# Kernel tuning notes

Hardware: AMD Instinct MI355X
Metric: run time of the kernel (lower is better)

The kernel has to match this reference:

```python
import jax, jax.numpy as jnp
import numpy as np

D = 256      # d_model
NH = 8       # num_heads
NP = 4       # n_points
H = 100      # feature map height (single level)
W = 100      # feature map width
B = 4
Q = H * W
S = H * W


def setup_inputs() -> dict:
    key = jax.random.key(0)
    ks = jax.random.split(key, 12)
    p = lambda k, shp, s=0.02: jax.random.normal(k, shp, jnp.float32) * s
    return {
        "hidden_states": jax.random.normal(ks[0], (B, Q, D), jnp.float32),
        "encoder_hidden_states": jax.random.normal(ks[1], (B, S, D), jnp.float32),
        "reference_points": jax.random.uniform(ks[2], (B, Q, 1, 2), jnp.float32),
        "spatial_shapes": jnp.array([[H, W]], dtype=jnp.int32),
        "W_off": p(ks[3], (NH * NP * 2, D)),
        "b_off": p(ks[4], (NH * NP * 2,), 0.5),
        "W_attn": p(ks[5], (NH * NP, D)),
        "b_attn": jnp.zeros((NH * NP,), jnp.float32),
        "W_val": p(ks[6], (D, D)),
        "b_val": jnp.zeros((D,), jnp.float32),
        "W_out": p(ks[7], (D, D)),
        "b_out": jnp.zeros((D,), jnp.float32),
    }


def _deform_attn(hidden_states, encoder_hidden_states, reference_points,
                 W_off, b_off, W_attn, b_attn, W_val, b_val, W_out, b_out):
    Bsz, Qn, Dm = hidden_states.shape
    d = Dm // NH

    # value projection -> [B, NH, S, d]
    value = (encoder_hidden_states @ W_val.T + b_val).reshape(Bsz, S, NH, d)
    vflat = value.transpose(0, 2, 1, 3).reshape(Bsz * NH, H * W, d)

    # sampling offsets [B,Q,NH,NP,2] (n_levels=1 squeezed)
    off = (hidden_states @ W_off.T + b_off).reshape(Bsz, Qn, NH, NP, 2)
    # attention weights softmax over (n_levels*n_points)=NP -> [B,Q,NH,NP]
    attn = jax.nn.softmax((hidden_states @ W_attn.T + b_attn).reshape(Bsz, Qn, NH, NP), axis=-1)

    # normalized sampling locations: ref + off / [W, H]
    normalizer = jnp.array([W, H], jnp.float32)
    # reference_points: [B,Q,1,2] (level dim) -> broadcast over heads/points
    loc = reference_points[:, :, None, 0, None, :] + off / normalizer  # [B,Q,NH,NP,2]

    # grid_sample semantics: grid = 2*loc - 1, align_corners=False, zeros padding
    gx = 2.0 * loc[..., 0] - 1.0
    gy = 2.0 * loc[..., 1] - 1.0
    x = ((gx + 1.0) * W - 1.0) * 0.5   # pixel coords [B,Q,NH,NP]
    y = ((gy + 1.0) * H - 1.0) * 0.5
    x0 = jnp.floor(x); y0 = jnp.floor(y)
    x1 = x0 + 1.0;     y1 = y0 + 1.0
    wx1 = x - x0; wx0 = 1.0 - wx1
    wy1 = y - y0; wy0 = 1.0 - wy1

    bh = jnp.arange(Bsz * NH)[:, None]

    def corner(xi, yi, wgt):
        valid = (xi >= 0) & (xi <= W - 1) & (yi >= 0) & (yi <= H - 1)
        xi_c = jnp.clip(xi, 0, W - 1).astype(jnp.int32)
        yi_c = jnp.clip(yi, 0, H - 1).astype(jnp.int32)
        idx = (yi_c * W + xi_c).transpose(0, 2, 1, 3).reshape(Bsz * NH, Qn * NP)
        g = vflat[bh, idx]  # [B*NH, Q*NP, d]
        wv = (wgt * valid.astype(wgt.dtype)).transpose(0, 2, 1, 3).reshape(Bsz * NH, Qn * NP, 1)
        return g * wv

    sampled = corner(x0, y0, wx0 * wy0)
    sampled = sampled + corner(x1, y0, wx1 * wy0)
    sampled = sampled + corner(x0, y1, wx0 * wy1)
    sampled = sampled + corner(x1, y1, wx1 * wy1)
    sampled = sampled.reshape(Bsz, NH, Qn, NP, d)

    out = jnp.einsum("bhqpd,bqhp->bqhd", sampled, attn).reshape(Bsz, Qn, Dm)
    return out @ W_out.T + b_out


def reference(hidden_states, encoder_hidden_states, reference_points, spatial_shapes,
              W_off, b_off, W_attn, b_attn, W_val, b_val, W_out, b_out):
    # spatial_shapes is static metadata (must equal [[H, W]]); shapes are baked in.
    return _deform_attn(hidden_states, encoder_hidden_states, reference_points,
                        W_off, b_off, W_attn, b_attn, W_val, b_val, W_out, b_out)
```

## Files before the change

### kernel.cpp

```cpp
#include <hip/hip_runtime.h>

constexpr int HH = 100;
constexpr int WW = 100;
constexpr int NH = 8;
constexpr int NP = 4;
constexpr int B  = 4;
constexpr int Q  = HH * WW;
constexpr int S  = Q;
constexpr int K  = 256;
constexpr int DH = 32;

typedef __attribute__((ext_vector_type(8))) short short8;
typedef __attribute__((ext_vector_type(4))) float f32x4;

struct ushort4_t { unsigned short x, y, z, w; };

__device__ inline unsigned short f2bf(float f) {
    unsigned u = __builtin_bit_cast(unsigned, f);
    u += 0x7fffu + ((u >> 16) & 1u);
    return (unsigned short)(u >> 16);
}
__device__ inline float bf2f(unsigned short h) {
    return __builtin_bit_cast(float, ((unsigned)h) << 16);
}

__device__ inline void lds_store16(short* base, int row, int kcol, short8 v) {
    const int idx = row * 64 + (kcol ^ ((row & 7) << 3));
    *reinterpret_cast<short8*>(&base[idx]) = v;
}
__device__ inline short8 lds_load16(const short* base, int row, int kcol) {
    const int idx = row * 64 + (kcol ^ ((row & 7) << 3));
    return *reinterpret_cast<const short8*>(&base[idx]);
}

__device__ inline short8 cvt8(float4 a, float4 b) {
    short8 r;
    r[0] = (short)f2bf(a.x); r[1] = (short)f2bf(a.y);
    r[2] = (short)f2bf(a.z); r[3] = (short)f2bf(a.w);
    r[4] = (short)f2bf(b.x); r[5] = (short)f2bf(b.y);
    r[6] = (short)f2bf(b.z); r[7] = (short)f2bf(b.w);
    return r;
}

template <int MODE, int NT>
__global__ __launch_bounds__(512) void gemm_mfma(
    const void* __restrict__ Ap, const float* __restrict__ W0,
    const float* __restrict__ W1, const float* __restrict__ b0,
    const float* __restrict__ b1, void* __restrict__ Cp, int N0)
{
    constexpr int BROWS = (NT + 63) / 64;

    __shared__ short As[64 * 64];
    __shared__ short Bs[NT * 64];

    const int tid  = threadIdx.x;
    const int m0   = blockIdx.x * 64;
    const int lane = tid & 63;
    const int w    = tid >> 6;
    const int l15  = lane & 15;
    const int l4   = lane >> 4;
    const int srow = tid >> 3;
    const int sk8  = (tid & 7) * 8;

    const int n_base = (MODE == 1) ? w * 16 : w * 32;
    constexpr int NF = (MODE == 1) ? 1 : 2;

    f32x4 acc[4][2];
#pragma unroll
    for (int i = 0; i < 4; ++i)
#pragma unroll
        for (int j = 0; j < 2; ++j)
            acc[i][j] = f32x4{0.f, 0.f, 0.f, 0.f};

    float4 fa0, fa1;
    short8 sa;
    float4 fb[BROWS][2];

    auto load_tile = [&](int k0) {
        if constexpr (MODE == 2) {
            const unsigned short* A = (const unsigned short*)Ap;
            sa = *reinterpret_cast<const short8*>(&A[(size_t)(m0 + srow) * K + k0 + sk8]);
        } else {
            const float* A = (const float*)Ap;
            const float* s = &A[(size_t)(m0 + srow) * K + k0 + sk8];
            fa0 = *reinterpret_cast<const float4*>(s);
            fa1 = *reinterpret_cast<const float4*>(s + 4);
        }
#pragma unroll
        for (int i = 0; i < BROWS; ++i) {
            const int row = srow + 64 * i;
            if ((NT % 64 == 0) || row < NT) {
                const float* s = (row < N0)
                    ? &W0[(size_t)row * K + k0 + sk8]
                    : &W1[(size_t)(row - N0) * K + k0 + sk8];
                fb[i][0] = *reinterpret_cast<const float4*>(s);
                fb[i][1] = *reinterpret_cast<const float4*>(s + 4);
            }
        }
    };
    auto write_lds = [&]() {
        if constexpr (MODE == 2) {
            lds_store16(As, srow, sk8, sa);
        } else {
            lds_store16(As, srow, sk8, cvt8(fa0, fa1));
        }
#pragma unroll
        for (int i = 0; i < BROWS; ++i) {
            const int row = srow + 64 * i;
            if ((NT % 64 == 0) || row < NT)
                lds_store16(Bs, row, sk8, cvt8(fb[i][0], fb[i][1]));
        }
    };

    load_tile(0);
    for (int k0 = 0; k0 < K; k0 += 64) {
        write_lds();
        __syncthreads();
        if (k0 + 64 < K) load_tile(k0 + 64);
        if (n_base < NT) {
#pragma unroll
            for (int kk = 0; kk < 2; ++kk) {
                const int kc = kk * 32 + l4 * 8;
                short8 a[4];
#pragma unroll
                for (int mf = 0; mf < 4; ++mf)
                    a[mf] = lds_load16(As, mf * 16 + l15, kc);
#pragma unroll
                for (int nf = 0; nf < NF; ++nf) {
                    const short8 bv = lds_load16(Bs, n_base + nf * 16 + l15, kc);
#pragma unroll
                    for (int mf = 0; mf < 4; ++mf)
                        acc[mf][nf] = __builtin_amdgcn_mfma_f32_16x16x32_bf16(
                            a[mf], bv, acc[mf][nf], 0, 0, 0);
                }
            }
        }
        __syncthreads();
    }

#pragma unroll
    for (int nf = 0; nf < NF; ++nf) {
        const int n = n_base + nf * 16 + l15;
        if (n >= NT) continue;
        const float bias = (n < N0) ? b0[n] : b1[n - N0];
#pragma unroll
        for (int mf = 0; mf < 4; ++mf) {
#pragma unroll
            for (int r = 0; r < 4; ++r) {
                const int m = m0 + mf * 16 + l4 * 4 + r;
                const float v = acc[mf][nf][r] + bias;
                if constexpr (MODE == 0) {
                    const int b = m / S, s = m - (m / S) * S;
                    const int h = n >> 5, dd = n & 31;
                    ((unsigned short*)Cp)[(((size_t)(b * NH + h)) * S + s) * DH + dd] = f2bf(v);
                } else if constexpr (MODE == 1) {
                    ((float*)Cp)[(size_t)m * 96 + n] = v;
                } else {
                    ((float*)Cp)[(size_t)m * 256 + n] = v;
                }
            }
        }
    }
}

__global__ __launch_bounds__(256) void sample_agg(
    const unsigned short* __restrict__ vflat,
    const float* __restrict__ proj,
    const float* __restrict__ ref,
    unsigned short* __restrict__ tmp)
{
    const int nblk = gridDim.x;
    const int cpx  = nblk >> 3;
    const int swz  = (blockIdx.x & 7) * cpx + (blockIdx.x >> 3);

    const int lg   = threadIdx.x >> 3;
    const int lane = threadIdx.x & 7;
    const int d0   = lane * 4;

    const int g  = swz * 32 + lg;
    const int q  = g % Q;
    const int bh = g / Q;
    const int b  = bh >> 3;
    const int h  = bh & 7;

    const size_t bq   = (size_t)b * Q + q;
    const float refx = ref[bq * 2 + 0];
    const float refy = ref[bq * 2 + 1];
    const float* pr = proj + bq * 96;

    float l[NP];
#pragma unroll
    for (int p = 0; p < NP; ++p) l[p] = pr[64 + h * 4 + p];
    const float mx = fmaxf(fmaxf(l[0], l[1]), fmaxf(l[2], l[3]));
    float e[NP];
    float esum = 0.f;
#pragma unroll
    for (int p = 0; p < NP; ++p) { e[p] = __expf(l[p] - mx); esum += e[p]; }
    const float inv = 1.f / esum;

    const unsigned short* vbase = vflat + (size_t)bh * (S * DH);

    int   cidx[NP][4];
    float cw[NP][4];
#pragma unroll
    for (int p = 0; p < NP; ++p) {
        const float ox = pr[h * 8 + p * 2 + 0];
        const float oy = pr[h * 8 + p * 2 + 1];
        const float x = (refx + ox * (1.0f / WW)) * WW - 0.5f;
        const float y = (refy + oy * (1.0f / HH)) * HH - 0.5f;
        const float x0f = floorf(x);
        const float y0f = floorf(y);
        const float wx1 = x - x0f, wx0 = 1.f - wx1;
        const float wy1 = y - y0f, wy0 = 1.f - wy1;
        const int x0 = (int)x0f;
        const int y0 = (int)y0f;
        const bool vx0 = (x0 >= 0) && (x0 <= WW - 1);
        const bool vx1 = (x0 + 1 >= 0) && (x0 + 1 <= WW - 1);
        const bool vy0 = (y0 >= 0) && (y0 <= HH - 1);
        const bool vy1 = (y0 + 1 >= 0) && (y0 + 1 <= HH - 1);
        const int xi0 = min(max(x0, 0), WW - 1);
        const int xi1 = min(max(x0 + 1, 0), WW - 1);
        const int yi0 = min(max(y0, 0), HH - 1);
        const int yi1 = min(max(y0 + 1, 0), HH - 1);
        const float ap = e[p] * inv;
        cw[p][0] = ap * wx0 * wy0 * ((vx0 && vy0) ? 1.f : 0.f);
        cw[p][1] = ap * wx1 * wy0 * ((vx1 && vy0) ? 1.f : 0.f);
        cw[p][2] = ap * wx0 * wy1 * ((vx0 && vy1) ? 1.f : 0.f);
        cw[p][3] = ap * wx1 * wy1 * ((vx1 && vy1) ? 1.f : 0.f);
        cidx[p][0] = (yi0 * WW + xi0) * DH + d0;
        cidx[p][1] = (yi0 * WW + xi1) * DH + d0;
        cidx[p][2] = (yi1 * WW + xi0) * DH + d0;
        cidx[p][3] = (yi1 * WW + xi1) * DH + d0;
    }

    float a0 = 0.f, a1 = 0.f, a2 = 0.f, a3 = 0.f;
#pragma unroll
    for (int p = 0; p < NP; ++p) {
#pragma unroll
        for (int c = 0; c < 4; ++c) {
            const ushort4_t v = *reinterpret_cast<const ushort4_t*>(&vbase[cidx[p][c]]);
            const float wgt = cw[p][c];
            a0 = fmaf(wgt, bf2f(v.x), a0);
            a1 = fmaf(wgt, bf2f(v.y), a1);
            a2 = fmaf(wgt, bf2f(v.z), a2);
            a3 = fmaf(wgt, bf2f(v.w), a3);
        }
    }

    ushort4_t o;
    o.x = f2bf(a0); o.y = f2bf(a1); o.z = f2bf(a2); o.w = f2bf(a3);
    *reinterpret_cast<ushort4_t*>(&tmp[bq * 256 + h * 32 + d0]) = o;
}

extern "C" void kernel_launch(void* const* d_in, const int* in_sizes, int n_in,
                              void* d_out, int out_size, void* d_ws, size_t ws_size,
                              hipStream_t stream)
{
    const float* hidden = (const float*)d_in[0];
    const float* enc    = (const float*)d_in[1];
    const float* refp   = (const float*)d_in[2];
    const float* W_off  = (const float*)d_in[4];
    const float* b_off  = (const float*)d_in[5];
    const float* W_attn = (const float*)d_in[6];
    const float* b_attn = (const float*)d_in[7];
    const float* W_val  = (const float*)d_in[8];
    const float* b_val  = (const float*)d_in[9];
    const float* W_out  = (const float*)d_in[10];
    const float* b_out  = (const float*)d_in[11];
    float* out = (float*)d_out;

    unsigned short* vflat = (unsigned short*)d_ws;
    float* proj = (float*)((char*)d_ws + (size_t)B * NH * S * DH * 2);
    unsigned short* tmp = (unsigned short*)((char*)proj + (size_t)B * Q * 96 * 4);

    const int M = B * Q;

    gemm_mfma<0, 256><<<M / 64, 512, 0, stream>>>(
        (const void*)enc, W_val, W_val, b_val, b_val, (void*)vflat, 256);

    gemm_mfma<1, 96><<<M / 64, 512, 0, stream>>>(
        (const void*)hidden, W_off, W_attn, b_off, b_attn, (void*)proj, 64);

    sample_agg<<<(B * NH * Q) / 32, 256, 0, stream>>>(vflat, proj, refp, tmp);

    gemm_mfma<2, 256><<<M / 64, 512, 0, stream>>>(
        (const void*)tmp, W_out, W_out, b_out, b_out, (void*)out, 256);
}
```

Baseline: 89.46 us.

## Fuse offset/attn projection, sampling and output projection into one kernel

Merges the offset/attention-logit GEMM, the bilinear sampling aggregation and the output projection into one per-64-row workgroup kernel. Intermediates (projections, packed corner indices and fp16 weights, aggregated rows) stay in LDS instead of going through global memory. The value projection becomes its own kernel with 32-row tiles. This removes two kernel launches and the global round-trips of proj and tmp. In exchange it uses 68 KB of dynamic LDS, which lowers occupancy, and stores intermediates in fp16, which loses some precision.

```diff
diff --git a/kernel.cpp b/kernel.cpp
--- a/kernel.cpp
+++ b/kernel.cpp
@@ -11,9 +11,10 @@
 constexpr int DH = 32;
 
 typedef __attribute__((ext_vector_type(8))) short short8;
+typedef __attribute__((ext_vector_type(4))) short short4_v;
 typedef __attribute__((ext_vector_type(4))) float f32x4;
 
-struct ushort4_t { unsigned short x, y, z, w; };
+struct __align__(8) ushort4_t { unsigned short x, y, z, w; };
 
 __device__ inline unsigned short f2bf(float f) {
     unsigned u = __builtin_bit_cast(unsigned, f);
@@ -23,14 +24,19 @@
 __device__ inline float bf2f(unsigned short h) {
     return __builtin_bit_cast(float, ((unsigned)h) << 16);
 }
-
-__device__ inline void lds_store16(short* base, int row, int kcol, short8 v) {
-    const int idx = row * 64 + (kcol ^ ((row & 7) << 3));
-    *reinterpret_cast<short8*>(&base[idx]) = v;
-}
-__device__ inline short8 lds_load16(const short* base, int row, int kcol) {
-    const int idx = row * 64 + (kcol ^ ((row & 7) << 3));
-    return *reinterpret_cast<const short8*>(&base[idx]);
+__device__ inline unsigned short f2h(float f) {
+    _Float16 h = (_Float16)f;
+    return __builtin_bit_cast(unsigned short, h);
+}
+__device__ inline float h2f(unsigned short u) {
+    return (float)__builtin_bit_cast(_Float16, u);
+}
+
+__device__ inline void lds_st16s(short* base, int row, int stride, int kcol, short8 v) {
+    *reinterpret_cast<short8*>(&base[row * stride + (kcol ^ ((row & 7) << 3))]) = v;
+}
+__device__ inline short8 lds_ld16s(const short* base, int row, int stride, int kcol) {
+    return *reinterpret_cast<const short8*>(&base[row * stride + (kcol ^ ((row & 7) << 3))]);
 }
 
 __device__ inline short8 cvt8(float4 a, float4 b) {
@@ -42,214 +48,311 @@
     return r;
 }
 
-template <int MODE, int NT>
-__global__ __launch_bounds__(512) void gemm_mfma(
-    const void* __restrict__ Ap, const float* __restrict__ W0,
-    const float* __restrict__ W1, const float* __restrict__ b0,
-    const float* __restrict__ b1, void* __restrict__ Cp, int N0)
+__global__ __launch_bounds__(512) void value_proj(
+    const float* __restrict__ enc, const float* __restrict__ Wv,
+    const float* __restrict__ bv, unsigned short* __restrict__ vflat)
 {
-    constexpr int BROWS = (NT + 63) / 64;
-
-    __shared__ short As[64 * 64];
-    __shared__ short Bs[NT * 64];
-
-    const int tid  = threadIdx.x;
-    const int m0   = blockIdx.x * 64;
-    const int lane = tid & 63;
-    const int w    = tid >> 6;
-    const int l15  = lane & 15;
-    const int l4   = lane >> 4;
-    const int srow = tid >> 3;
-    const int sk8  = (tid & 7) * 8;
-
-    const int n_base = (MODE == 1) ? w * 16 : w * 32;
-    constexpr int NF = (MODE == 1) ? 1 : 2;
-
-    f32x4 acc[4][2];
-#pragma unroll
-    for (int i = 0; i < 4; ++i)
-#pragma unroll
-        for (int j = 0; j < 2; ++j)
-            acc[i][j] = f32x4{0.f, 0.f, 0.f, 0.f};
-
-    float4 fa0, fa1;
-    short8 sa;
-    float4 fb[BROWS][2];
-
-    auto load_tile = [&](int k0) {
-        if constexpr (MODE == 2) {
-            const unsigned short* A = (const unsigned short*)Ap;
-            sa = *reinterpret_cast<const short8*>(&A[(size_t)(m0 + srow) * K + k0 + sk8]);
-        } else {
-            const float* A = (const float*)Ap;
-            const float* s = &A[(size_t)(m0 + srow) * K + k0 + sk8];
-            fa0 = *reinterpret_cast<const float4*>(s);
-            fa1 = *reinterpret_cast<const float4*>(s + 4);
-        }
-#pragma unroll
-        for (int i = 0; i < BROWS; ++i) {
-            const int row = srow + 64 * i;
-            if ((NT % 64 == 0) || row < NT) {
-                const float* s = (row < N0)
-                    ? &W0[(size_t)row * K + k0 + sk8]
-                    : &W1[(size_t)(row - N0) * K + k0 + sk8];
-                fb[i][0] = *reinterpret_cast<const float4*>(s);
-                fb[i][1] = *reinterpret_cast<const float4*>(s + 4);
-            }
+    __shared__ short As[32 * 64];
+    __shared__ short Bs[256 * 64];
+
+    const int tid = threadIdx.x;
+    const int m0  = blockIdx.x * 32;
+    const int lane = tid & 63, w = tid >> 6;
+    const int l15 = lane & 15, l4 = lane >> 4;
+
+    const int arow = tid >> 4, ak4 = (tid & 15) * 4;
+    const int brow = tid >> 1, bk32 = (tid & 1) * 32;
+
+    f32x4 acc[2][2];
+#pragma unroll
+    for (int i = 0; i < 2; ++i)
+#pragma unroll
+        for (int j = 0; j < 2; ++j) acc[i][j] = f32x4{0.f, 0.f, 0.f, 0.f};
+
+    for (int k0 = 0; k0 < K; k0 += 64) {
+        {
+            float4 f = *reinterpret_cast<const float4*>(
+                &enc[(size_t)(m0 + arow) * K + k0 + ak4]);
+            short4_v s;
+            s[0] = (short)f2bf(f.x); s[1] = (short)f2bf(f.y);
+            s[2] = (short)f2bf(f.z); s[3] = (short)f2bf(f.w);
+            *reinterpret_cast<short4_v*>(&As[arow * 64 + (ak4 ^ ((arow & 7) << 3))]) = s;
+        }
+        {
+            const float* src = &Wv[(size_t)brow * K + k0 + bk32];
+#pragma unroll
+            for (int c = 0; c < 4; ++c) {
+                float4 f0 = *reinterpret_cast<const float4*>(src + c * 8);
+                float4 f1 = *reinterpret_cast<const float4*>(src + c * 8 + 4);
+                lds_st16s(Bs, brow, 64, bk32 + c * 8, cvt8(f0, f1));
+            }
+        }
+        __syncthreads();
+#pragma unroll
+        for (int kk = 0; kk < 2; ++kk) {
+            const int kc = kk * 32 + l4 * 8;
+            short8 a0 = lds_ld16s(As, l15, 64, kc);
+            short8 a1 = lds_ld16s(As, 16 + l15, 64, kc);
+#pragma unroll
+            for (int nf = 0; nf < 2; ++nf) {
+                short8 bb = lds_ld16s(Bs, w * 32 + nf * 16 + l15, 64, kc);
+                acc[0][nf] = __builtin_amdgcn_mfma_f32_16x16x32_bf16(a0, bb, acc[0][nf], 0, 0, 0);
+                acc[1][nf] = __builtin_amdgcn_mfma_f32_16x16x32_bf16(a1, bb, acc[1][nf], 0, 0, 0);
+            }
+        }
+        __syncthreads();
+    }
+
+#pragma unroll
+    for (int nf = 0; nf < 2; ++nf) {
+        const int n = w * 32 + nf * 16 + l15;
+        const float bias = bv[n];
+        const int h = n >> 5, dd = n & 31;
+#pragma unroll
+        for (int mf = 0; mf < 2; ++mf) {
+#pragma unroll
+            for (int r = 0; r < 4; ++r) {
+                const int m = m0 + mf * 16 + l4 * 4 + r;
+                const int b = m / S, s = m - (m / S) * S;
+                vflat[(((size_t)(b * NH + h)) * S + s) * DH + dd] =
+                    f2bf(acc[mf][nf][r] + bias);
+            }
+        }
+    }
+}
+
+__global__ __launch_bounds__(512) void fused_dsa(
+    const float* __restrict__ hidden, const float* __restrict__ W_off,
+    const float* __restrict__ W_attn, const float* __restrict__ b_off,
+    const float* __restrict__ b_attn, const float* __restrict__ ref,
+    const unsigned short* __restrict__ vflat, const float* __restrict__ W_out,
+    const float* __restrict__ b_out, float* __restrict__ out)
+{
+    extern __shared__ char smem[];
+    unsigned short* P   = (unsigned short*)smem;
+    unsigned int*   cidx = (unsigned int*)(smem + 12288);
+    uint2*          cw   = (uint2*)(smem + 20480);
+    short* tmpB = (short*)(smem + 36864);
+    short* As   = (short*)(smem + 36864);
+    short* Bs   = (short*)(smem + 45056);
+    short* Ws   = (short*)smem;
+
+    const int nwg = gridDim.x;
+    const int q8 = nwg >> 3, r8 = nwg & 7;
+    const int xcd = blockIdx.x & 7, pos = blockIdx.x >> 3;
+    const int start = (xcd < r8) ? xcd * (q8 + 1) : r8 * (q8 + 1) + (xcd - r8) * q8;
+    const int m0 = (start + pos) * 64;
+
+    const int tid = threadIdx.x;
+    const int lane = tid & 63, w = tid >> 6;
+    const int l15 = lane & 15, l4 = lane >> 4;
+
+    const int srow = tid >> 3, sk8 = (tid & 7) * 8;
+    const bool bstage2 = (srow < 32);
+    const int brow2 = 64 + srow;
+
+    f32x4 acc1[4];
+#pragma unroll
+    for (int i = 0; i < 4; ++i) acc1[i] = f32x4{0.f, 0.f, 0.f, 0.f};
+    const int nb1 = w * 16;
+
+    float4 fa0, fa1, fb00, fb01, fb10, fb11;
+    auto ld1 = [&](int k0) {
+        const float* s = &hidden[(size_t)(m0 + srow) * K + k0 + sk8];
+        fa0 = *reinterpret_cast<const float4*>(s);
+        fa1 = *reinterpret_cast<const float4*>(s + 4);
+        const float* s0 = &W_off[(size_t)srow * K + k0 + sk8];
+        fb00 = *reinterpret_cast<const float4*>(s0);
+        fb01 = *reinterpret_cast<const float4*>(s0 + 4);
+        if (bstage2) {
+            const float* s1 = &W_attn[(size_t)srow * K + k0 + sk8];
+            fb10 = *reinterpret_cast<const float4*>(s1);
+            fb11 = *reinterpret_cast<const float4*>(s1 + 4);
         }
     };
-    auto write_lds = [&]() {
-        if constexpr (MODE == 2) {
-            lds_store16(As, srow, sk8, sa);
-        } else {
-            lds_store16(As, srow, sk8, cvt8(fa0, fa1));
-        }
-#pragma unroll
-        for (int i = 0; i < BROWS; ++i) {
-            const int row = srow + 64 * i;
-            if ((NT % 64 == 0) || row < NT)
-                lds_store16(Bs, row, sk8, cvt8(fb[i][0], fb[i][1]));
-        }
+    auto wr1 = [&]() {
+        lds_st16s(As, srow, 64, sk8, cvt8(fa0, fa1));
+        lds_st16s(Bs, srow, 64, sk8, cvt8(fb00, fb01));
+        if (bstage2) lds_st16s(Bs, brow2, 64, sk8, cvt8(fb10, fb11));
     };
 
-    load_tile(0);
+    ld1(0);
     for (int k0 = 0; k0 < K; k0 += 64) {
-        write_lds();
-        __syncthreads();
-        if (k0 + 64 < K) load_tile(k0 + 64);
-        if (n_base < NT) {
+        wr1();
+        __syncthreads();
+        if (k0 < K - 64) ld1(k0 + 64);
+        if (w < 6) {
 #pragma unroll
             for (int kk = 0; kk < 2; ++kk) {
                 const int kc = kk * 32 + l4 * 8;
                 short8 a[4];
 #pragma unroll
                 for (int mf = 0; mf < 4; ++mf)
-                    a[mf] = lds_load16(As, mf * 16 + l15, kc);
-#pragma unroll
-                for (int nf = 0; nf < NF; ++nf) {
-                    const short8 bv = lds_load16(Bs, n_base + nf * 16 + l15, kc);
-#pragma unroll
-                    for (int mf = 0; mf < 4; ++mf)
-                        acc[mf][nf] = __builtin_amdgcn_mfma_f32_16x16x32_bf16(
-                            a[mf], bv, acc[mf][nf], 0, 0, 0);
-                }
-            }
-        }
-        __syncthreads();
-    }
-
-#pragma unroll
-    for (int nf = 0; nf < NF; ++nf) {
-        const int n = n_base + nf * 16 + l15;
-        if (n >= NT) continue;
-        const float bias = (n < N0) ? b0[n] : b1[n - N0];
-#pragma unroll
-        for (int mf = 0; mf < 4; ++mf) {
+                    a[mf] = lds_ld16s(As, mf * 16 + l15, 64, kc);
+                short8 bb = lds_ld16s(Bs, nb1 + l15, 64, kc);
+#pragma unroll
+                for (int mf = 0; mf < 4; ++mf)
+                    acc1[mf] = __builtin_amdgcn_mfma_f32_16x16x32_bf16(a[mf], bb, acc1[mf], 0, 0, 0);
+            }
+        }
+        __syncthreads();
+    }
+    if (w < 6) {
+        const int col = nb1 + l15;
+        const float bias = (col < 64) ? b_off[col] : b_attn[col - 64];
+#pragma unroll
+        for (int mf = 0; mf < 4; ++mf)
 #pragma unroll
             for (int r = 0; r < 4; ++r) {
-                const int m = m0 + mf * 16 + l4 * 4 + r;
-                const float v = acc[mf][nf][r] + bias;
-                if constexpr (MODE == 0) {
-                    const int b = m / S, s = m - (m / S) * S;
-                    const int h = n >> 5, dd = n & 31;
-                    ((unsigned short*)Cp)[(((size_t)(b * NH + h)) * S + s) * DH + dd] = f2bf(v);
-                } else if constexpr (MODE == 1) {
-                    ((float*)Cp)[(size_t)m * 96 + n] = v;
-                } else {
-                    ((float*)Cp)[(size_t)m * 256 + n] = v;
-                }
-            }
-        }
-    }
-}
-
-__global__ __launch_bounds__(256) void sample_agg(
-    const unsigned short* __restrict__ vflat,
-    const float* __restrict__ proj,
-    const float* __restrict__ ref,
-    unsigned short* __restrict__ tmp)
-{
-    const int nblk = gridDim.x;
-    const int cpx  = nblk >> 3;
-    const int swz  = (blockIdx.x & 7) * cpx + (blockIdx.x >> 3);
-
-    const int lg   = threadIdx.x >> 3;
-    const int lane = threadIdx.x & 7;
-    const int d0   = lane * 4;
-
-    const int g  = swz * 32 + lg;
-    const int q  = g % Q;
-    const int bh = g / Q;
-    const int b  = bh >> 3;
-    const int h  = bh & 7;
-
-    const size_t bq   = (size_t)b * Q + q;
-    const float refx = ref[bq * 2 + 0];
-    const float refy = ref[bq * 2 + 1];
-    const float* pr = proj + bq * 96;
-
-    float l[NP];
-#pragma unroll
-    for (int p = 0; p < NP; ++p) l[p] = pr[64 + h * 4 + p];
-    const float mx = fmaxf(fmaxf(l[0], l[1]), fmaxf(l[2], l[3]));
-    float e[NP];
-    float esum = 0.f;
-#pragma unroll
-    for (int p = 0; p < NP; ++p) { e[p] = __expf(l[p] - mx); esum += e[p]; }
-    const float inv = 1.f / esum;
-
-    const unsigned short* vbase = vflat + (size_t)bh * (S * DH);
-
-    int   cidx[NP][4];
-    float cw[NP][4];
-#pragma unroll
-    for (int p = 0; p < NP; ++p) {
-        const float ox = pr[h * 8 + p * 2 + 0];
-        const float oy = pr[h * 8 + p * 2 + 1];
-        const float x = (refx + ox * (1.0f / WW)) * WW - 0.5f;
-        const float y = (refy + oy * (1.0f / HH)) * HH - 0.5f;
-        const float x0f = floorf(x);
-        const float y0f = floorf(y);
-        const float wx1 = x - x0f, wx0 = 1.f - wx1;
-        const float wy1 = y - y0f, wy0 = 1.f - wy1;
-        const int x0 = (int)x0f;
-        const int y0 = (int)y0f;
-        const bool vx0 = (x0 >= 0) && (x0 <= WW - 1);
-        const bool vx1 = (x0 + 1 >= 0) && (x0 + 1 <= WW - 1);
-        const bool vy0 = (y0 >= 0) && (y0 <= HH - 1);
-        const bool vy1 = (y0 + 1 >= 0) && (y0 + 1 <= HH - 1);
-        const int xi0 = min(max(x0, 0), WW - 1);
-        const int xi1 = min(max(x0 + 1, 0), WW - 1);
-        const int yi0 = min(max(y0, 0), HH - 1);
-        const int yi1 = min(max(y0 + 1, 0), HH - 1);
-        const float ap = e[p] * inv;
-        cw[p][0] = ap * wx0 * wy0 * ((vx0 && vy0) ? 1.f : 0.f);
-        cw[p][1] = ap * wx1 * wy0 * ((vx1 && vy0) ? 1.f : 0.f);
-        cw[p][2] = ap * wx0 * wy1 * ((vx0 && vy1) ? 1.f : 0.f);
-        cw[p][3] = ap * wx1 * wy1 * ((vx1 && vy1) ? 1.f : 0.f);
-        cidx[p][0] = (yi0 * WW + xi0) * DH + d0;
-        cidx[p][1] = (yi0 * WW + xi1) * DH + d0;
-        cidx[p][2] = (yi1 * WW + xi0) * DH + d0;
-        cidx[p][3] = (yi1 * WW + xi1) * DH + d0;
-    }
-
-    float a0 = 0.f, a1 = 0.f, a2 = 0.f, a3 = 0.f;
-#pragma unroll
-    for (int p = 0; p < NP; ++p) {
-#pragma unroll
-        for (int c = 0; c < 4; ++c) {
-            const ushort4_t v = *reinterpret_cast<const ushort4_t*>(&vbase[cidx[p][c]]);
-            const float wgt = cw[p][c];
-            a0 = fmaf(wgt, bf2f(v.x), a0);
-            a1 = fmaf(wgt, bf2f(v.y), a1);
-            a2 = fmaf(wgt, bf2f(v.z), a2);
-            a3 = fmaf(wgt, bf2f(v.w), a3);
-        }
-    }
-
-    ushort4_t o;
-    o.x = f2bf(a0); o.y = f2bf(a1); o.z = f2bf(a2); o.w = f2bf(a3);
-    *reinterpret_cast<ushort4_t*>(&tmp[bq * 256 + h * 32 + d0]) = o;
+                const int row = mf * 16 + l4 * 4 + r;
+                P[row * 96 + col] = f2h(acc1[mf][r] + bias);
+            }
+    }
+    __syncthreads();
+
+    {
+        const int r = tid >> 3, h = tid & 7;
+        const int m = m0 + r;
+        const float refx = ref[(size_t)m * 2 + 0];
+        const float refy = ref[(size_t)m * 2 + 1];
+        float l[NP];
+#pragma unroll
+        for (int p = 0; p < NP; ++p) l[p] = h2f(P[r * 96 + 64 + h * 4 + p]);
+        const float mx = fmaxf(fmaxf(l[0], l[1]), fmaxf(l[2], l[3]));
+        float e[NP]; float esum = 0.f;
+#pragma unroll
+        for (int p = 0; p < NP; ++p) { e[p] = __expf(l[p] - mx); esum += e[p]; }
+        const float inv = 1.f / esum;
+#pragma unroll
+        for (int p = 0; p < NP; ++p) {
+            const float ox = h2f(P[r * 96 + h * 8 + p * 2 + 0]);
+            const float oy = h2f(P[r * 96 + h * 8 + p * 2 + 1]);
+            const float x = fmaf(refx, (float)WW, ox) - 0.5f;
+            const float y = fmaf(refy, (float)HH, oy) - 0.5f;
+            const float x0f = floorf(x), y0f = floorf(y);
+            const float wx1 = x - x0f, wx0 = 1.f - wx1;
+            const float wy1 = y - y0f, wy0 = 1.f - wy1;
+            const int x0 = (int)x0f, y0 = (int)y0f;
+            const bool vx0 = (x0 >= 0) && (x0 < WW);
+            const bool vx1 = (x0 + 1 >= 0) && (x0 + 1 < WW);
+            const bool vy0 = (y0 >= 0) && (y0 < HH);
+            const bool vy1 = (y0 + 1 >= 0) && (y0 + 1 < HH);
+            const int xi0 = min(max(x0, 0), WW - 1);
+            const int xi1 = min(max(x0 + 1, 0), WW - 1);
+            const int yi0 = min(max(y0, 0), HH - 1);
+            const int yi1 = min(max(y0 + 1, 0), HH - 1);
+            const float ap = e[p] * inv;
+            const float c0 = ap * wx0 * wy0 * ((vx0 && vy0) ? 1.f : 0.f);
+            const float c1 = ap * wx1 * wy0 * ((vx1 && vy0) ? 1.f : 0.f);
+            const float c2 = ap * wx0 * wy1 * ((vx0 && vy1) ? 1.f : 0.f);
+            const float c3 = ap * wx1 * wy1 * ((vx1 && vy1) ? 1.f : 0.f);
+            const int trip = ((r * 8 + h) << 2) + p;
+            cidx[trip] = (unsigned)xi0 | ((unsigned)xi1 << 8)
+                       | ((unsigned)yi0 << 16) | ((unsigned)yi1 << 24);
+            uint2 wv;
+            wv.x = (unsigned)f2h(c0) | ((unsigned)f2h(c1) << 16);
+            wv.y = (unsigned)f2h(c2) | ((unsigned)f2h(c3) << 16);
+            cw[trip] = wv;
+        }
+    }
+    __syncthreads();
+
+    {
+        const int r = tid >> 3, d0 = (tid & 7) * 4;
+        const int m = m0 + r;
+        const int b = m / Q;
+        float o[8][4];
+#pragma unroll
+        for (int h = 0; h < 8; ++h)
+#pragma unroll
+            for (int c = 0; c < 4; ++c) o[h][c] = 0.f;
+
+#pragma unroll
+        for (int h = 0; h < 8; ++h) {
+            const unsigned short* vb = vflat + (size_t)(b * NH + h) * (S * DH);
+#pragma unroll
+            for (int p = 0; p < NP; ++p) {
+                const int trip = ((r * 8 + h) << 2) + p;
+                const unsigned u = cidx[trip];
+                const uint2 wv = cw[trip];
+                const int xi0 = u & 255, xi1 = (u >> 8) & 255;
+                const int yi0 = (u >> 16) & 255, yi1 = u >> 24;
+                const float c0 = h2f((unsigned short)(wv.x & 0xffff));
+                const float c1 = h2f((unsigned short)(wv.x >> 16));
+                const float c2 = h2f((unsigned short)(wv.y & 0xffff));
+                const float c3 = h2f((unsigned short)(wv.y >> 16));
+                const ushort4_t v0 = *reinterpret_cast<const ushort4_t*>(&vb[(size_t)((yi0 * WW + xi0) * DH + d0)]);
+                const ushort4_t v1 = *reinterpret_cast<const ushort4_t*>(&vb[(size_t)((yi0 * WW + xi1) * DH + d0)]);
+                const ushort4_t v2 = *reinterpret_cast<const ushort4_t*>(&vb[(size_t)((yi1 * WW + xi0) * DH + d0)]);
+                const ushort4_t v3 = *reinterpret_cast<const ushort4_t*>(&vb[(size_t)((yi1 * WW + xi1) * DH + d0)]);
+                o[h][0] = fmaf(c0, bf2f(v0.x), fmaf(c1, bf2f(v1.x), fmaf(c2, bf2f(v2.x), fmaf(c3, bf2f(v3.x), o[h][0]))));
+                o[h][1] = fmaf(c0, bf2f(v0.y), fmaf(c1, bf2f(v1.y), fmaf(c2, bf2f(v2.y), fmaf(c3, bf2f(v3.y), o[h][1]))));
+                o[h][2] = fmaf(c0, bf2f(v0.z), fmaf(c1, bf2f(v1.z), fmaf(c2, bf2f(v2.z), fmaf(c3, bf2f(v3.z), o[h][2]))));
+                o[h][3] = fmaf(c0, bf2f(v0.w), fmaf(c1, bf2f(v1.w), fmaf(c2, bf2f(v2.w), fmaf(c3, bf2f(v3.w), o[h][3]))));
+            }
+        }
+#pragma unroll
+        for (int h = 0; h < 8; ++h) {
+            const int c = h * 32 + d0;
+            const int idx = r * 256 + (c ^ ((r & 7) << 3));
+            ushort4_t ov;
+            ov.x = f2bf(o[h][0]); ov.y = f2bf(o[h][1]);
+            ov.z = f2bf(o[h][2]); ov.w = f2bf(o[h][3]);
+            *reinterpret_cast<ushort4_t*>(&tmpB[idx]) = ov;
+        }
+    }
+    __syncthreads();
+
+    f32x4 acc2[4][2];
+#pragma unroll
+    for (int i = 0; i < 4; ++i)
+#pragma unroll
+        for (int j = 0; j < 2; ++j) acc2[i][j] = f32x4{0.f, 0.f, 0.f, 0.f};
+
+    const int wrow = tid >> 1, wk32 = (tid & 1) * 32;
+    const int nb3 = w * 32;
+
+    for (int k0 = 0; k0 < K; k0 += 64) {
+        {
+            const float* s = &W_out[(size_t)wrow * K + k0 + wk32];
+#pragma unroll
+            for (int c = 0; c < 4; ++c) {
+                float4 f0 = *reinterpret_cast<const float4*>(s + c * 8);
+                float4 f1 = *reinterpret_cast<const float4*>(s + c * 8 + 4);
+                lds_st16s(Ws, wrow, 64, wk32 + c * 8, cvt8(f0, f1));
+            }
+        }
+        __syncthreads();
+#pragma unroll
+        for (int kk = 0; kk < 2; ++kk) {
+            const int kc = kk * 32 + l4 * 8;
+            short8 a[4];
+#pragma unroll
+            for (int mf = 0; mf < 4; ++mf)
+                a[mf] = lds_ld16s(tmpB, mf * 16 + l15, 256, k0 + kc);
+#pragma unroll
+            for (int nf = 0; nf < 2; ++nf) {
+                short8 bb = lds_ld16s(Ws, nb3 + nf * 16 + l15, 64, kc);
+#pragma unroll
+                for (int mf = 0; mf < 4; ++mf)
+                    acc2[mf][nf] = __builtin_amdgcn_mfma_f32_16x16x32_bf16(a[mf], bb, acc2[mf][nf], 0, 0, 0);
+            }
+        }
+        __syncthreads();
+    }
+
+#pragma unroll
+    for (int nf = 0; nf < 2; ++nf) {
+        const int n = nb3 + nf * 16 + l15;
+        const float bias = b_out[n];
+#pragma unroll
+        for (int mf = 0; mf < 4; ++mf)
+#pragma unroll
+            for (int r = 0; r < 4; ++r) {
+                const int mrow = m0 + mf * 16 + l4 * 4 + r;
+                out[(size_t)mrow * K + n] = acc2[mf][nf][r] + bias;
+            }
+    }
 }
 
 extern "C" void kernel_launch(void* const* d_in, const int* in_sizes, int n_in,
@@ -270,19 +373,11 @@
     float* out = (float*)d_out;
 
     unsigned short* vflat = (unsigned short*)d_ws;
-    float* proj = (float*)((char*)d_ws + (size_t)B * NH * S * DH * 2);
-    unsigned short* tmp = (unsigned short*)((char*)proj + (size_t)B * Q * 96 * 4);
 
     const int M = B * Q;
 
-    gemm_mfma<0, 256><<<M / 64, 512, 0, stream>>>(
-        (const void*)enc, W_val, W_val, b_val, b_val, (void*)vflat, 256);
-
-    gemm_mfma<1, 96><<<M / 64, 512, 0, stream>>>(
-        (const void*)hidden, W_off, W_attn, b_off, b_attn, (void*)proj, 64);
-
-    sample_agg<<<(B * NH * Q) / 32, 256, 0, stream>>>(vflat, proj, refp, tmp);
-
-    gemm_mfma<2, 256><<<M / 64, 512, 0, stream>>>(
-        (const void*)tmp, W_out, W_out, b_out, b_out, (void*)out, 256);
-}
+    value_proj<<<M / 32, 512, 0, stream>>>(enc, W_val, b_val, vflat);
+
+    fused_dsa<<<M / 64, 512, 69632, stream>>>(
+        hidden, W_off, W_attn, b_off, b_attn, refp, vflat, W_out, b_out, out);
+}
```

Result: slower. 131.5 us (+47.0%).

## Merge value and offset projections into one launch, split output GEMM over N

Applied to the files above, without the earlier changes.

The value-projection GEMM and the offset/attention projection GEMM are merged into a single launch. The first 625 blocks handle the value projection and the rest handle the offset/attention projection, so the two independent GEMMs run concurrently and one launch disappears. The output projection becomes its own kernel that splits N into two 128-column halves, doubling the grid to 1250 blocks with smaller per-block LDS and accumulators to improve occupancy. The trade-off is heterogeneous blocks within one grid and the A tile being loaded twice in the output GEMM.

```diff
diff --git a/kernel.cpp b/kernel.cpp
--- a/kernel.cpp
+++ b/kernel.cpp
@@ -13,7 +13,7 @@
 typedef __attribute__((ext_vector_type(8))) short short8;
 typedef __attribute__((ext_vector_type(4))) float f32x4;
 
-struct ushort4_t { unsigned short x, y, z, w; };
+struct __align__(8) ushort4_t { unsigned short x, y, z, w; };
 
 __device__ inline unsigned short f2bf(float f) {
     unsigned u = __builtin_bit_cast(unsigned, f);
@@ -24,13 +24,11 @@
     return __builtin_bit_cast(float, ((unsigned)h) << 16);
 }
 
-__device__ inline void lds_store16(short* base, int row, int kcol, short8 v) {
-    const int idx = row * 64 + (kcol ^ ((row & 7) << 3));
-    *reinterpret_cast<short8*>(&base[idx]) = v;
-}
-__device__ inline short8 lds_load16(const short* base, int row, int kcol) {
-    const int idx = row * 64 + (kcol ^ ((row & 7) << 3));
-    return *reinterpret_cast<const short8*>(&base[idx]);
+__device__ inline void lds_st16s(short* base, int row, int kcol, short8 v) {
+    *reinterpret_cast<short8*>(&base[row * 64 + (kcol ^ ((row & 7) << 3))]) = v;
+}
+__device__ inline short8 lds_ld16s(const short* base, int row, int kcol) {
+    return *reinterpret_cast<const short8*>(&base[row * 64 + (kcol ^ ((row & 7) << 3))]);
 }
 
 __device__ inline short8 cvt8(float4 a, float4 b) {
@@ -42,123 +40,150 @@
     return r;
 }
 
-template <int MODE, int NT>
-__global__ __launch_bounds__(512) void gemm_mfma(
-    const void* __restrict__ Ap, const float* __restrict__ W0,
-    const float* __restrict__ W1, const float* __restrict__ b0,
-    const float* __restrict__ b1, void* __restrict__ Cp, int N0)
+__global__ __launch_bounds__(512) void dual_gemm(
+    const float* __restrict__ enc, const float* __restrict__ Wval,
+    const float* __restrict__ bval, unsigned short* __restrict__ vflat,
+    const float* __restrict__ hidden, const float* __restrict__ Woff,
+    const float* __restrict__ Wattn, const float* __restrict__ boff,
+    const float* __restrict__ battn, float* __restrict__ proj)
 {
-    constexpr int BROWS = (NT + 63) / 64;
-
     __shared__ short As[64 * 64];
-    __shared__ short Bs[NT * 64];
+    __shared__ short Bs[256 * 64];
 
     const int tid  = threadIdx.x;
-    const int m0   = blockIdx.x * 64;
-    const int lane = tid & 63;
-    const int w    = tid >> 6;
-    const int l15  = lane & 15;
-    const int l4   = lane >> 4;
-    const int srow = tid >> 3;
-    const int sk8  = (tid & 7) * 8;
-
-    const int n_base = (MODE == 1) ? w * 16 : w * 32;
-    constexpr int NF = (MODE == 1) ? 1 : 2;
-
-    f32x4 acc[4][2];
-#pragma unroll
-    for (int i = 0; i < 4; ++i)
-#pragma unroll
-        for (int j = 0; j < 2; ++j)
-            acc[i][j] = f32x4{0.f, 0.f, 0.f, 0.f};
-
-    float4 fa0, fa1;
-    short8 sa;
-    float4 fb[BROWS][2];
-
-    auto load_tile = [&](int k0) {
-        if constexpr (MODE == 2) {
-            const unsigned short* A = (const unsigned short*)Ap;
-            sa = *reinterpret_cast<const short8*>(&A[(size_t)(m0 + srow) * K + k0 + sk8]);
-        } else {
-            const float* A = (const float*)Ap;
-            const float* s = &A[(size_t)(m0 + srow) * K + k0 + sk8];
+    const int lane = tid & 63, w = tid >> 6;
+    const int l15  = lane & 15, l4 = lane >> 4;
+    const int srow = tid >> 3, sk8 = (tid & 7) * 8;
+
+    if (blockIdx.x < 625) {
+        const int m0 = blockIdx.x * 64;
+        const int n_base = w * 32;
+
+        f32x4 acc[4][2];
+#pragma unroll
+        for (int i = 0; i < 4; ++i)
+#pragma unroll
+            for (int j = 0; j < 2; ++j) acc[i][j] = f32x4{0.f, 0.f, 0.f, 0.f};
+
+        float4 fa0, fa1;
+        float4 fb[4][2];
+        auto ld = [&](int k0) {
+            const float* s = &enc[(size_t)(m0 + srow) * K + k0 + sk8];
             fa0 = *reinterpret_cast<const float4*>(s);
             fa1 = *reinterpret_cast<const float4*>(s + 4);
-        }
-#pragma unroll
-        for (int i = 0; i < BROWS; ++i) {
-            const int row = srow + 64 * i;
-            if ((NT % 64 == 0) || row < NT) {
-                const float* s = (row < N0)
-                    ? &W0[(size_t)row * K + k0 + sk8]
-                    : &W1[(size_t)(row - N0) * K + k0 + sk8];
-                fb[i][0] = *reinterpret_cast<const float4*>(s);
-                fb[i][1] = *reinterpret_cast<const float4*>(s + 4);
-            }
-        }
-    };
-    auto write_lds = [&]() {
-        if constexpr (MODE == 2) {
-            lds_store16(As, srow, sk8, sa);
-        } else {
-            lds_store16(As, srow, sk8, cvt8(fa0, fa1));
-        }
-#pragma unroll
-        for (int i = 0; i < BROWS; ++i) {
-            const int row = srow + 64 * i;
-            if ((NT % 64 == 0) || row < NT)
-                lds_store16(Bs, row, sk8, cvt8(fb[i][0], fb[i][1]));
-        }
-    };
-
-    load_tile(0);
-    for (int k0 = 0; k0 < K; k0 += 64) {
-        write_lds();
-        __syncthreads();
-        if (k0 + 64 < K) load_tile(k0 + 64);
-        if (n_base < NT) {
+#pragma unroll
+            for (int i = 0; i < 4; ++i) {
+                const float* ws = &Wval[(size_t)(srow + 64 * i) * K + k0 + sk8];
+                fb[i][0] = *reinterpret_cast<const float4*>(ws);
+                fb[i][1] = *reinterpret_cast<const float4*>(ws + 4);
+            }
+        };
+        auto wr = [&]() {
+            lds_st16s(As, srow, sk8, cvt8(fa0, fa1));
+#pragma unroll
+            for (int i = 0; i < 4; ++i)
+                lds_st16s(Bs, srow + 64 * i, sk8, cvt8(fb[i][0], fb[i][1]));
+        };
+
+        ld(0);
+        for (int k0 = 0; k0 < K; k0 += 64) {
+            wr();
+            __syncthreads();
+            if (k0 < K - 64) ld(k0 + 64);
 #pragma unroll
             for (int kk = 0; kk < 2; ++kk) {
                 const int kc = kk * 32 + l4 * 8;
                 short8 a[4];
 #pragma unroll
                 for (int mf = 0; mf < 4; ++mf)
-                    a[mf] = lds_load16(As, mf * 16 + l15, kc);
-#pragma unroll
-                for (int nf = 0; nf < NF; ++nf) {
-                    const short8 bv = lds_load16(Bs, n_base + nf * 16 + l15, kc);
+                    a[mf] = lds_ld16s(As, mf * 16 + l15, kc);
+#pragma unroll
+                for (int nf = 0; nf < 2; ++nf) {
+                    const short8 bv = lds_ld16s(Bs, n_base + nf * 16 + l15, kc);
 #pragma unroll
                     for (int mf = 0; mf < 4; ++mf)
                         acc[mf][nf] = __builtin_amdgcn_mfma_f32_16x16x32_bf16(
                             a[mf], bv, acc[mf][nf], 0, 0, 0);
                 }
             }
-        }
-        __syncthreads();
-    }
-
-#pragma unroll
-    for (int nf = 0; nf < NF; ++nf) {
-        const int n = n_base + nf * 16 + l15;
-        if (n >= NT) continue;
-        const float bias = (n < N0) ? b0[n] : b1[n - N0];
-#pragma unroll
-        for (int mf = 0; mf < 4; ++mf) {
-#pragma unroll
-            for (int r = 0; r < 4; ++r) {
-                const int m = m0 + mf * 16 + l4 * 4 + r;
-                const float v = acc[mf][nf][r] + bias;
-                if constexpr (MODE == 0) {
+            __syncthreads();
+        }
+
+#pragma unroll
+        for (int nf = 0; nf < 2; ++nf) {
+            const int n = n_base + nf * 16 + l15;
+            const float bias = bval[n];
+            const int h = n >> 5, dd = n & 31;
+#pragma unroll
+            for (int mf = 0; mf < 4; ++mf)
+#pragma unroll
+                for (int r = 0; r < 4; ++r) {
+                    const int m = m0 + mf * 16 + l4 * 4 + r;
                     const int b = m / S, s = m - (m / S) * S;
-                    const int h = n >> 5, dd = n & 31;
-                    ((unsigned short*)Cp)[(((size_t)(b * NH + h)) * S + s) * DH + dd] = f2bf(v);
-                } else if constexpr (MODE == 1) {
-                    ((float*)Cp)[(size_t)m * 96 + n] = v;
-                } else {
-                    ((float*)Cp)[(size_t)m * 256 + n] = v;
+                    vflat[(((size_t)(b * NH + h)) * S + s) * DH + dd] =
+                        f2bf(acc[mf][nf][r] + bias);
                 }
-            }
+        }
+    } else {
+        const int m0 = (blockIdx.x - 625) * 64;
+        const int n_base = w * 16;
+
+        f32x4 acc[4];
+#pragma unroll
+        for (int i = 0; i < 4; ++i) acc[i] = f32x4{0.f, 0.f, 0.f, 0.f};
+
+        float4 fa0, fa1;
+        float4 fb[2][2];
+        const int row1 = srow + 64;
+        auto ld = [&](int k0) {
+            const float* s = &hidden[(size_t)(m0 + srow) * K + k0 + sk8];
+            fa0 = *reinterpret_cast<const float4*>(s);
+            fa1 = *reinterpret_cast<const float4*>(s + 4);
+            const float* w0 = &Woff[(size_t)srow * K + k0 + sk8];
+            fb[0][0] = *reinterpret_cast<const float4*>(w0);
+            fb[0][1] = *reinterpret_cast<const float4*>(w0 + 4);
+            if (row1 < 96) {
+                const float* w1 = &Wattn[(size_t)(row1 - 64) * K + k0 + sk8];
+                fb[1][0] = *reinterpret_cast<const float4*>(w1);
+                fb[1][1] = *reinterpret_cast<const float4*>(w1 + 4);
+            }
+        };
+        auto wr = [&]() {
+            lds_st16s(As, srow, sk8, cvt8(fa0, fa1));
+            lds_st16s(Bs, srow, sk8, cvt8(fb[0][0], fb[0][1]));
+            if (row1 < 96) lds_st16s(Bs, row1, sk8, cvt8(fb[1][0], fb[1][1]));
+        };
+
+        ld(0);
+        for (int k0 = 0; k0 < K; k0 += 64) {
+            wr();
+            __syncthreads();
+            if (k0 < K - 64) ld(k0 + 64);
+            if (w < 6) {
+#pragma unroll
+                for (int kk = 0; kk < 2; ++kk) {
+                    const int kc = kk * 32 + l4 * 8;
+                    const short8 bv = lds_ld16s(Bs, n_base + l15, kc);
+#pragma unroll
+                    for (int mf = 0; mf < 4; ++mf) {
+                        const short8 a = lds_ld16s(As, mf * 16 + l15, kc);
+                        acc[mf] = __builtin_amdgcn_mfma_f32_16x16x32_bf16(
+                            a, bv, acc[mf], 0, 0, 0);
+                    }
+                }
+            }
+            __syncthreads();
+        }
+        if (w < 6) {
+            const int col = n_base + l15;
+            const float bias = (col < 64) ? boff[col] : battn[col - 64];
+#pragma unroll
+            for (int mf = 0; mf < 4; ++mf)
+#pragma unroll
+                for (int r = 0; r < 4; ++r) {
+                    const int m = m0 + mf * 16 + l4 * 4 + r;
+                    proj[(size_t)m * 96 + col] = acc[mf][r] + bias;
+                }
         }
     }
 }
@@ -208,16 +233,14 @@
         const float oy = pr[h * 8 + p * 2 + 1];
         const float x = (refx + ox * (1.0f / WW)) * WW - 0.5f;
         const float y = (refy + oy * (1.0f / HH)) * HH - 0.5f;
-        const float x0f = floorf(x);
-        const float y0f = floorf(y);
+        const float x0f = floorf(x), y0f = floorf(y);
         const float wx1 = x - x0f, wx0 = 1.f - wx1;
         const float wy1 = y - y0f, wy0 = 1.f - wy1;
-        const int x0 = (int)x0f;
-        const int y0 = (int)y0f;
-        const bool vx0 = (x0 >= 0) && (x0 <= WW - 1);
-        const bool vx1 = (x0 + 1 >= 0) && (x0 + 1 <= WW - 1);
-        const bool vy0 = (y0 >= 0) && (y0 <= HH - 1);
-        const bool vy1 = (y0 + 1 >= 0) && (y0 + 1 <= HH - 1);
+        const int x0 = (int)x0f, y0 = (int)y0f;
+        const bool vx0 = (x0 >= 0) && (x0 < WW);
+        const bool vx1 = (x0 + 1 >= 0) && (x0 + 1 < WW);
+        const bool vy0 = (y0 >= 0) && (y0 < HH);
+        const bool vy1 = (y0 + 1 >= 0) && (y0 + 1 < HH);
         const int xi0 = min(max(x0, 0), WW - 1);
         const int xi1 = min(max(x0 + 1, 0), WW - 1);
         const int yi0 = min(max(y0, 0), HH - 1);
@@ -250,6 +273,75 @@
     ushort4_t o;
     o.x = f2bf(a0); o.y = f2bf(a1); o.z = f2bf(a2); o.w = f2bf(a3);
     *reinterpret_cast<ushort4_t*>(&tmp[bq * 256 + h * 32 + d0]) = o;
+}
+
+__global__ __launch_bounds__(512) void out_proj(
+    const unsigned short* __restrict__ tmp, const float* __restrict__ Wo,
+    const float* __restrict__ bo, float* __restrict__ out)
+{
+    __shared__ short As[64 * 64];
+    __shared__ short Bs[128 * 64];
+
+    const int bid = blockIdx.x;
+    const int m0  = (bid >> 1) * 64;
+    const int n0  = (bid & 1) * 128;
+
+    const int tid  = threadIdx.x;
+    const int lane = tid & 63, w = tid >> 6;
+    const int l15  = lane & 15, l4 = lane >> 4;
+    const int srow = tid >> 3, sk8 = (tid & 7) * 8;
+
+    f32x4 acc[4];
+#pragma unroll
+    for (int i = 0; i < 4; ++i) acc[i] = f32x4{0.f, 0.f, 0.f, 0.f};
+
+    short8 sa;
+    float4 fb[2][2];
+    auto ld = [&](int k0) {
+        sa = *reinterpret_cast<const short8*>(
+            &tmp[(size_t)(m0 + srow) * K + k0 + sk8]);
+#pragma unroll
+        for (int i = 0; i < 2; ++i) {
+            const float* ws = &Wo[(size_t)(n0 + srow + 64 * i) * K + k0 + sk8];
+            fb[i][0] = *reinterpret_cast<const float4*>(ws);
+            fb[i][1] = *reinterpret_cast<const float4*>(ws + 4);
+        }
+    };
+    auto wr = [&]() {
+        lds_st16s(As, srow, sk8, sa);
+#pragma unroll
+        for (int i = 0; i < 2; ++i)
+            lds_st16s(Bs, srow + 64 * i, sk8, cvt8(fb[i][0], fb[i][1]));
+    };
+
+    ld(0);
+    for (int k0 = 0; k0 < K; k0 += 64) {
+        wr();
+        __syncthreads();
+        if (k0 < K - 64) ld(k0 + 64);
+#pragma unroll
+        for (int kk = 0; kk < 2; ++kk) {
+            const int kc = kk * 32 + l4 * 8;
+            const short8 bv = lds_ld16s(Bs, w * 16 + l15, kc);
+#pragma unroll
+            for (int mf = 0; mf < 4; ++mf) {
+                const short8 a = lds_ld16s(As, mf * 16 + l15, kc);
+                acc[mf] = __builtin_amdgcn_mfma_f32_16x16x32_bf16(
+                    a, bv, acc[mf], 0, 0, 0);
+            }
+        }
+        __syncthreads();
+    }
+
+    const int n = n0 + w * 16 + l15;
+    const float bias = bo[n];
+#pragma unroll
+    for (int mf = 0; mf < 4; ++mf)
+#pragma unroll
+        for (int r = 0; r < 4; ++r) {
+            const int m = m0 + mf * 16 + l4 * 4 + r;
+            out[(size_t)m * K + n] = acc[mf][r] + bias;
+        }
 }
 
 extern "C" void kernel_launch(void* const* d_in, const int* in_sizes, int n_in,
@@ -275,14 +367,10 @@
 
     const int M = B * Q;
 
-    gemm_mfma<0, 256><<<M / 64, 512, 0, stream>>>(
-        (const void*)enc, W_val, W_val, b_val, b_val, (void*)vflat, 256);
-
-    gemm_mfma<1, 96><<<M / 64, 512, 0, stream>>>(
-        (const void*)hidden, W_off, W_attn, b_off, b_attn, (void*)proj, 64);
+    dual_gemm<<<1250, 512, 0, stream>>>(
+        enc, W_val, b_val, vflat, hidden, W_off, W_attn, b_off, b_attn, proj);
 
     sample_agg<<<(B * NH * Q) / 32, 256, 0, stream>>>(vflat, proj, refp, tmp);
 
-    gemm_mfma<2, 256><<<M / 64, 512, 0, stream>>>(
-        (const void*)tmp, W_out, W_out, b_out, b_out, (void*)out, 256);
-}
+    out_proj<<<1250, 512, 0, stream>>>(tmp, W_out, b_out, out);
+}
```

New measurement: 79.39 us. 1.13x faster.
